# Performance work log

Hardware: AMD Instinct MI355X
Metric: run time of the kernel (lower is better)

Reference implementation:

```python
import jax, jax.numpy as jnp
import numpy as np

B, T, C = 4, 2048, 1024
NH = 16
HS = C // NH


def setup_inputs() -> dict:
    key = jax.random.key(0)
    k1, k2, k3, k4, k5 = jax.random.split(key, 5)
    scale = 1.0 / np.sqrt(C)
    return {
        "x": jax.random.normal(k1, (B, T, C), dtype=jnp.float32),
        "Wk": jax.random.normal(k2, (C, C), dtype=jnp.float32) * scale,
        "Wq": jax.random.normal(k3, (C, C), dtype=jnp.float32) * scale,
        "Wv": jax.random.normal(k4, (C, C), dtype=jnp.float32) * scale,
        "Wp": jax.random.normal(k5, (C, C), dtype=jnp.float32) * scale,
    }


def reference(x, Wk, Wq, Wv, Wp):
    b, t, c = x.shape
    # projections (nn.Linear with bias=False computes x @ W.T; weights here are
    # stored so that x @ W is equivalent -- same math, random init either way)
    k = (x @ Wk).reshape(b, t, NH, HS).transpose(0, 2, 1, 3)  # [B,H,T,hs]
    q = (x @ Wq).reshape(b, t, NH, HS).transpose(0, 2, 1, 3)
    v = (x @ Wv).reshape(b, t, NH, HS).transpose(0, 2, 1, 3)
    att = jnp.einsum("bhqd,bhkd->bhqk", q, k) / jnp.sqrt(jnp.float32(HS))
    causal = jnp.tril(jnp.ones((t, t), dtype=bool))
    att = jnp.where(causal[None, None, :, :], att, -jnp.inf)
    att = jax.nn.softmax(att, axis=-1)
    y = jnp.einsum("bhqk,bhkd->bhqd", att, v)  # [B,H,T,hs]
    y = y.transpose(0, 2, 1, 3).reshape(b, t, c)
    return y @ Wp
```

## Files before the change

### kernel.cpp

```cpp
#include <hip/hip_runtime.h>
#include <cstddef>
#include <cstdint>


namespace {

typedef unsigned short u16;
typedef unsigned int u32;
typedef __attribute__((ext_vector_type(8))) short s8v;
typedef __attribute__((ext_vector_type(4))) short s4v;
typedef __attribute__((ext_vector_type(4))) float f4v;

constexpr int Bn = 4, Tn = 2048, Cn = 1024;
constexpr int Mn = Bn * Tn;
constexpr int KVB = 128;
constexpr int NT128 = Tn / 128;
constexpr float QSCALE = 0.125f * 1.44269504f;

__device__ __forceinline__ u16 bfc(float f) {
  return __builtin_bit_cast(u16, (__bf16)f);
}

__device__ __forceinline__ f4v mfma16(s8v a, s8v b, f4v c) {
  return __builtin_amdgcn_mfma_f32_16x16x32_bf16(a, b, c, 0, 0, 0);
}

__device__ __forceinline__ f4v mfma16k16(s4v a, s4v b, f4v c) {
#if __has_builtin(__builtin_amdgcn_mfma_f32_16x16x16bf16_1k)
  return __builtin_amdgcn_mfma_f32_16x16x16bf16_1k(a, b, c, 0, 0, 0);
#else
  f4v d = c;
  asm("v_mfma_f32_16x16x16_bf16 %0, %1, %2, %0" : "+v"(d) : "v"(a), "v"(b));
  return d;
#endif
}

typedef __attribute__((address_space(1))) const u32 gas_u32;
typedef __attribute__((address_space(3))) u32 las_u32;
__device__ __forceinline__ void gl_lds16(const void* g, void* l) {
  __builtin_amdgcn_global_load_lds((gas_u32*)g, (las_u32*)l, 16, 0, 0);
}

__global__ __launch_bounds__(256) void cvtx(const float* __restrict__ in,
                                            u16* __restrict__ out) {
  const size_t i = ((size_t)blockIdx.x * 256 + threadIdx.x) * 8;
  const float4 a = *(const float4*)(in + i);
  const float4 b = *(const float4*)(in + i + 4);
  alignas(16) u16 t[8] = {bfc(a.x), bfc(a.y), bfc(a.z), bfc(a.w),
                          bfc(b.x), bfc(b.y), bfc(b.z), bfc(b.w)};
  *(s8v*)(out + i) = *(const s8v*)t;
}

__global__ __launch_bounds__(256) void wtrans(
    const float* __restrict__ w0, const float* __restrict__ w1,
    const float* __restrict__ w2, const float* __restrict__ w3,
    u16* __restrict__ o0, u16* __restrict__ o1, u16* __restrict__ o2,
    u16* __restrict__ o3) {
  const float* W;
  u16* O;
  switch (blockIdx.z) {
    case 0: W = w0; O = o0; break;
    case 1: W = w1; O = o1; break;
    case 2: W = w2; O = o2; break;
    default: W = w3; O = o3; break;
  }
  __shared__ float Tsh[64][65];
  const int tid = threadIdx.x;
  const int n0 = blockIdx.x * 64, k0 = blockIdx.y * 64;
  {
    const int rk = tid >> 2, c0 = (tid & 3) * 16;
#pragma unroll
    for (int u = 0; u < 4; ++u) {
      const float4 v = *(const float4*)&W[(size_t)(k0 + rk) * Cn + n0 + c0 + u * 4];
      Tsh[rk][c0 + u * 4 + 0] = v.x;
      Tsh[rk][c0 + u * 4 + 1] = v.y;
      Tsh[rk][c0 + u * 4 + 2] = v.z;
      Tsh[rk][c0 + u * 4 + 3] = v.w;
    }
  }
  __syncthreads();
  {
    const int rn = tid >> 2, ck0 = (tid & 3) * 16;
    alignas(16) u16 t[16];
#pragma unroll
    for (int u = 0; u < 16; ++u) t[u] = bfc(Tsh[ck0 + u][rn]);
    *(s8v*)&O[(size_t)(n0 + rn) * Cn + k0 + ck0] = *(const s8v*)&t[0];
    *(s8v*)&O[(size_t)(n0 + rn) * Cn + k0 + ck0 + 8] = *(const s8v*)&t[8];
  }
}

template <int OUT_MODE>
__device__ __forceinline__ void gemm_body(const u16* __restrict__ A,
                                          const u16* __restrict__ Bt,
                                          void* __restrict__ Cout, int bm,
                                          int bn, u16* As, u16* Bs) {
  const int N = Cn, K = Cn;
  const int tid = threadIdx.x;
  const int l = tid & 63, w = tid >> 6;
  const int lr = l & 15, lh = l >> 4;
  const int lrow = tid >> 2;
  const int lkcol = (tid & 3) * 8;
  const u16* Ag = A + (size_t)(bm * 128 + lrow) * K + lkcol;
  const u16* Bg = Bt + (size_t)(bn * 128 + lrow) * K + lkcol;
  const int wm = (w >> 1) * 64, wn = (w & 1) * 64;
  f4v acc[4][4] = {};
  for (int k0 = 0; k0 < K; k0 += 32) {
    __syncthreads();
    gl_lds16(Ag + k0, &As[(size_t)tid * 8]);
    gl_lds16(Ag + (size_t)64 * K + k0, &As[2048 + (size_t)tid * 8]);
    gl_lds16(Bg + k0, &Bs[(size_t)tid * 8]);
    gl_lds16(Bg + (size_t)64 * K + k0, &Bs[2048 + (size_t)tid * 8]);
    __syncthreads();
    s8v af[4], bfr[4];
#pragma unroll
    for (int i = 0; i < 4; ++i)
      af[i] = *(const s8v*)&As[(wm + i * 16 + lr) * 32 + lh * 8];
#pragma unroll
    for (int j = 0; j < 4; ++j)
      bfr[j] = *(const s8v*)&Bs[(wn + j * 16 + lr) * 32 + lh * 8];
    __builtin_amdgcn_s_setprio(1);
#pragma unroll
    for (int i = 0; i < 4; ++i)
#pragma unroll
      for (int j = 0; j < 4; ++j)
        acc[i][j] = mfma16(af[i], bfr[j], acc[i][j]);
    __builtin_amdgcn_s_setprio(0);
  }
  if (OUT_MODE == 2) {
    float* Cf = (float*)Cout;
#pragma unroll
    for (int i = 0; i < 4; ++i) {
      const int row = bm * 128 + wm + i * 16 + lh * 4;
#pragma unroll
      for (int j = 0; j < 4; ++j) {
        const int col = bn * 128 + wn + j * 16 + lr;
#pragma unroll
        for (int r = 0; r < 4; ++r)
          Cf[(size_t)(row + r) * N + col] = acc[i][j][r];
      }
    }
  } else if (OUT_MODE == 0 || OUT_MODE == 3) {
    u16* Cb = (u16*)Cout;
    const float sc = (OUT_MODE == 3) ? QSCALE : 1.0f;
#pragma unroll
    for (int i = 0; i < 4; ++i) {
      const int row = bm * 128 + wm + i * 16 + lh * 4;
#pragma unroll
      for (int j = 0; j < 4; ++j) {
        const int col = bn * 128 + wn + j * 16 + lr;
#pragma unroll
        for (int r = 0; r < 4; ++r)
          Cb[(size_t)(row + r) * N + col] = bfc(acc[i][j][r] * sc);
      }
    }
  } else {
    u16* Vt = (u16*)Cout;
#pragma unroll
    for (int i = 0; i < 4; ++i) {
      const int row0 = bm * 128 + wm + i * 16 + lh * 4;
      const int bq = row0 >> 11, t0 = row0 & 2047;
#pragma unroll
      for (int j = 0; j < 4; ++j) {
        const int col = bn * 128 + wn + j * 16 + lr;
        const int hh = col >> 6, dd = col & 63;
        alignas(8) u16 t4[4];
#pragma unroll
        for (int r = 0; r < 4; ++r) t4[r] = bfc(acc[i][j][r]);
        *(s4v*)&Vt[((size_t)((bq * 16 + hh) * 64 + dd)) * Tn + t0] =
            *(const s4v*)t4;
      }
    }
  }
}

__global__ __launch_bounds__(256) void gemm_qkv(
    const u16* __restrict__ A, const u16* __restrict__ btq,
    const u16* __restrict__ btk, const u16* __restrict__ btv,
    u16* __restrict__ qb, u16* __restrict__ kb, u16* __restrict__ vt) {
  __shared__ __align__(16) u16 As[4096], Bs[4096];
  const int bid = blockIdx.x;
  const int wg = (bid & 7) * 192 + (bid >> 3);
  const int which = wg >> 9, inner = wg & 511;
  const int bm = inner & 63, bn = inner >> 6;
  if (which == 0)
    gemm_body<3>(A, btq, qb, bm, bn, As, Bs);
  else if (which == 1)
    gemm_body<0>(A, btk, kb, bm, bn, As, Bs);
  else
    gemm_body<1>(A, btv, vt, bm, bn, As, Bs);
}

template <int OUT_MODE>
__global__ __launch_bounds__(256) void gemm_bt(const u16* __restrict__ A,
                                               const u16* __restrict__ Bt,
                                               void* __restrict__ Cout) {
  __shared__ __align__(16) u16 As[4096], Bs[4096];
  const int bid = blockIdx.x;
  const int wg = (bid & 7) * 64 + (bid >> 3);
  const int bm = wg & 63, bn = wg >> 6;
  gemm_body<OUT_MODE>(A, Bt, Cout, bm, bn, As, Bs);
}

__device__ __forceinline__ void attn_step(const s8v* aq, const u16* Ks,
                                          const u16* Vs, int ln, int w,
                                          int lr, int lh, bool diag, int k0,
                                          int q0, float& m_i, float& l_i,
                                          f4v* o) {
  f4v s[8] = {};
  {
    const int sw = lr & 7;
    __builtin_amdgcn_s_setprio(1);
#pragma unroll
    for (int n = 0; n < 8; ++n) {
      const int rk = n * 16 + lr;
#pragma unroll
      for (int kd = 0; kd < 2; ++kd) {
        const s8v bk = *(const s8v*)&Ks[rk * 64 + (((kd * 4 + lh) ^ sw) * 8)];
        s[n] = mfma16(bk, aq[kd], s[n]);
      }
    }
    __builtin_amdgcn_s_setprio(0);
  }
  const int qg = q0 + w * 16 + lr;
  float rm = -1e30f;
  if (diag) {
#pragma unroll
    for (int n = 0; n < 8; ++n)
#pragma unroll
      for (int r = 0; r < 4; ++r) {
        float x = s[n][r];
        if (k0 + n * 16 + lh * 4 + r > qg) x = -1e30f;
        s[n][r] = x;
        rm = fmaxf(rm, x);
      }
  } else {
#pragma unroll
    for (int n = 0; n < 8; ++n)
#pragma unroll
      for (int r = 0; r < 4; ++r) rm = fmaxf(rm, s[n][r]);
  }
  rm = fmaxf(rm, __shfl_xor(rm, 16));
  rm = fmaxf(rm, __shfl_xor(rm, 32));
  if (!__all(rm <= m_i + 11.5f)) {
    const float mnew = fmaxf(m_i, rm);
    const float al = exp2f(m_i - mnew);
    m_i = mnew;
    l_i *= al;
#pragma unroll
    for (int r = 0; r < 4; ++r) {
      const float ar = __shfl(al, (ln & 48) | (lh * 4 + r));
#pragma unroll
      for (int n2 = 0; n2 < 4; ++n2) o[n2][r] *= ar;
    }
  }
  float rs = 0.f;
#pragma unroll
  for (int n = 0; n < 8; ++n) {
    const float p0 = exp2f(s[n][0] - m_i);
    const float p1 = exp2f(s[n][1] - m_i);
    const float p2 = exp2f(s[n][2] - m_i);
    const float p3 = exp2f(s[n][3] - m_i);
    rs += (p0 + p1) + (p2 + p3);
    const s4v pa = {(short)bfc(p0), (short)bfc(p1), (short)bfc(p2),
                    (short)bfc(p3)};
    __builtin_amdgcn_s_setprio(1);
#pragma unroll
    for (int n2 = 0; n2 < 4; ++n2) {
      const int d = n2 * 16 + lr;
      const int cl = (2 * n + (lh >> 1)) ^ (lr & 7);
      const s4v bv = *(const s4v*)&Vs[d * 128 + cl * 8 + (lh & 1) * 4];
      o[n2] = mfma16k16(pa, bv, o[n2]);
    }
    __builtin_amdgcn_s_setprio(0);
  }
  rs += __shfl_xor(rs, 16);
  rs += __shfl_xor(rs, 32);
  l_i += rs;
}

__global__ __launch_bounds__(512) void attn_big(const u16* __restrict__ qg,
                                                const u16* __restrict__ kg,
                                                const u16* __restrict__ vtg,
                                                u16* __restrict__ yg) {
  __shared__ __align__(16) u16 Ks[KVB * 64];
  __shared__ __align__(16) u16 Vs[64 * KVB];
  const int tid = threadIdx.x;
  const int ln = tid & 63, w = tid >> 6;
  const int lr = ln & 15, lh = ln >> 4;
  const int bid = blockIdx.x;
  const int wg = (bid & 7) * 64 + (bid >> 3);
  const int bh = wg >> 3, xp = wg & 7;
  const int b = bh >> 4, h = bh & 15;
  const int tL = xp, tH = NT128 - 1 - xp;
  const int q0L = tL * 128, q0H = tH * 128;
  s8v aqL[2], aqH[2];
  {
    const int row = w * 16 + lr;
#pragma unroll
    for (int kd = 0; kd < 2; ++kd) {
      aqL[kd] = *(const s8v*)&qg[(size_t)(b * Tn + q0L + row) * Cn + h * 64 +
                                 kd * 32 + lh * 8];
      aqH[kd] = *(const s8v*)&qg[(size_t)(b * Tn + q0H + row) * Cn + h * 64 +
                                 kd * 32 + lh * 8];
    }
  }
  float mL = -1e30f, lL = 0.f, mH = -1e30f, lH = 0.f;
  f4v oL[4] = {}, oH[4] = {};
  const int krr0 = tid >> 3, krc = (tid & 7) * 8;
  const int vrr0 = tid >> 4, vrc = (tid & 15) * 8;
  s8v kr0, kr1, vr0, vr1;
  {
    kr0 = *(const s8v*)&kg[(size_t)(b * Tn + krr0) * Cn + h * 64 + krc];
    kr1 = *(const s8v*)&kg[(size_t)(b * Tn + 64 + krr0) * Cn + h * 64 + krc];
    vr0 = *(const s8v*)&vtg[((size_t)(bh * 64 + vrr0)) * Tn + vrc];
    vr1 = *(const s8v*)&vtg[((size_t)(bh * 64 + 32 + vrr0)) * Tn + vrc];
  }
  for (int kt = 0; kt <= tH; ++kt) {
    __syncthreads();
    {
      const int c = tid & 7;
      *(s8v*)&Ks[krr0 * 64 + ((c ^ (krr0 & 7)) * 8)] = kr0;
      *(s8v*)&Ks[(64 + krr0) * 64 + ((c ^ ((64 + krr0) & 7)) * 8)] = kr1;
      const int cv = tid & 15;
      *(s8v*)&Vs[vrr0 * 128 + ((cv ^ (vrr0 & 7)) * 8)] = vr0;
      *(s8v*)&Vs[(32 + vrr0) * 128 + ((cv ^ ((32 + vrr0) & 7)) * 8)] = vr1;
    }
    __syncthreads();
    if (kt < tH) {
      const int k0n = (kt + 1) * KVB;
      kr0 = *(const s8v*)&kg[(size_t)(b * Tn + k0n + krr0) * Cn + h * 64 + krc];
      kr1 = *(const s8v*)&kg[(size_t)(b * Tn + k0n + 64 + krr0) * Cn + h * 64 + krc];
      vr0 = *(const s8v*)&vtg[((size_t)(bh * 64 + vrr0)) * Tn + k0n + vrc];
      vr1 = *(const s8v*)&vtg[((size_t)(bh * 64 + 32 + vrr0)) * Tn + k0n + vrc];
    }
    attn_step(aqH, Ks, Vs, ln, w, lr, lh, kt == tH, kt * KVB, q0H, mH, lH, oH);
    if (kt <= tL)
      attn_step(aqL, Ks, Vs, ln, w, lr, lh, kt == tL, kt * KVB, q0L, mL, lL,
                oL);
  }
  {
    const float linv = 1.0f / lH;
#pragma unroll
    for (int r = 0; r < 4; ++r) {
      const float iv = __shfl(linv, (ln & 48) | (lh * 4 + r));
      const int row = q0H + w * 16 + lh * 4 + r;
#pragma unroll
      for (int n2 = 0; n2 < 4; ++n2)
        yg[(size_t)(b * Tn + row) * Cn + h * 64 + n2 * 16 + lr] =
            bfc(oH[n2][r] * iv);
    }
  }
  {
    const float linv = 1.0f / lL;
#pragma unroll
    for (int r = 0; r < 4; ++r) {
      const float iv = __shfl(linv, (ln & 48) | (lh * 4 + r));
      const int row = q0L + w * 16 + lh * 4 + r;
#pragma unroll
      for (int n2 = 0; n2 < 4; ++n2)
        yg[(size_t)(b * Tn + row) * Cn + h * 64 + n2 * 16 + lr] =
            bfc(oL[n2][r] * iv);
    }
  }
}

}

extern "C" void kernel_launch(void* const* d_in, const int* in_sizes, int n_in,
                              void* d_out, int out_size, void* d_ws,
                              size_t ws_size, hipStream_t stream) {
  (void)in_sizes; (void)n_in; (void)out_size; (void)ws_size;
  const float* x = (const float*)d_in[0];
  const float* Wk = (const float*)d_in[1];
  const float* Wq = (const float*)d_in[2];
  const float* Wv = (const float*)d_in[3];
  const float* Wp = (const float*)d_in[4];
  float* out = (float*)d_out;
  char* ws = (char*)d_ws;

  u16* xb = (u16*)(ws);
  u16* wqt = (u16*)(ws + 16777216);
  u16* wkt = (u16*)(ws + 18874368);
  u16* wvt = (u16*)(ws + 20971520);
  u16* wpt = (u16*)(ws + 23068672);
  u16* qb = (u16*)(ws + 25165824);
  u16* kb = (u16*)(ws + 41943040);
  u16* vt = (u16*)(ws + 58720256);
  u16* yb = (u16*)(ws + 75497472);

  cvtx<<<dim3(4096), dim3(256), 0, stream>>>(x, xb);
  wtrans<<<dim3(16, 16, 4), dim3(256), 0, stream>>>(Wq, Wk, Wv, Wp, wqt, wkt,
                                                    wvt, wpt);
  gemm_qkv<<<dim3(1536), dim3(256), 0, stream>>>(xb, wqt, wkt, wvt, qb, kb,
                                                 vt);
  attn_big<<<dim3(512), dim3(512), 0, stream>>>(qb, kb, vt, yb);
  gemm_bt<2><<<dim3(512), dim3(256), 0, stream>>>(yb, wpt, out);
}
```

Measured before the change: 209.1 us.

## Double-buffer K/V tiles with direct global-to-LDS loads and defer softmax reductions

Replaces the register-staged K/V load with double-buffered LDS tiles filled by direct global-to-LDS copies, so the next tile loads while the current one is computed and one barrier per iteration is dropped. Moves the row-sum cross-lane reduction to the epilogue and does the max shuffle only when a rescale is needed. Switches to the hardware exp2 intrinsic and adds an occupancy hint to launch bounds. Doubling LDS use may reduce occupancy, and the deferred per-lane max check changes when rescales happen.

```diff
diff --git a/kernel.cpp b/kernel.cpp
--- a/kernel.cpp
+++ b/kernel.cpp
@@ -19,6 +19,14 @@
 
 __device__ __forceinline__ u16 bfc(float f) {
   return __builtin_bit_cast(u16, (__bf16)f);
+}
+
+__device__ __forceinline__ float ex2(float x) {
+#if __has_builtin(__builtin_amdgcn_exp2f)
+  return __builtin_amdgcn_exp2f(x);
+#else
+  return exp2f(x);
+#endif
 }
 
 __device__ __forceinline__ f4v mfma16(s8v a, s8v b, f4v c) {
@@ -201,11 +209,32 @@
   gemm_body<OUT_MODE>(A, Bt, Cout, bm, bn, As, Bs);
 }
 
-__device__ __forceinline__ void attn_step(const s8v* aq, const u16* Ks,
-                                          const u16* Vs, int ln, int w,
-                                          int lr, int lh, bool diag, int k0,
-                                          int q0, float& m_i, float& l_i,
-                                          f4v* o) {
+__device__ __forceinline__ void stage_kv(const u16* __restrict__ kgb,
+                                         const u16* __restrict__ vtb,
+                                         u16* __restrict__ Kb,
+                                         u16* __restrict__ Vb, int k0,
+                                         int tid) {
+#pragma unroll
+  for (int is = 0; is < 2; ++is) {
+    const int slot = is * 512 + tid;
+    const int row = slot >> 3, ch = slot & 7;
+    gl_lds16(kgb + (size_t)(k0 + row) * Cn + ((ch ^ (row & 7)) * 8),
+             &Kb[slot * 8]);
+  }
+#pragma unroll
+  for (int is = 0; is < 2; ++is) {
+    const int slot = is * 512 + tid;
+    const int d = slot >> 4, ch = slot & 15;
+    gl_lds16(vtb + (size_t)d * Tn + k0 + ((ch ^ (d & 7)) * 8), &Vb[slot * 8]);
+  }
+}
+
+__device__ __forceinline__ void attn_step(const s8v* aq,
+                                          const u16* __restrict__ Ks,
+                                          const u16* __restrict__ Vs, int ln,
+                                          int w, int lr, int lh, bool diag,
+                                          int k0, int q0, float& m_i,
+                                          float& l_i, f4v* o) {
   f4v s[8] = {};
   {
     const int sw = lr & 7;
@@ -236,14 +265,13 @@
   } else {
 #pragma unroll
     for (int n = 0; n < 8; ++n)
-#pragma unroll
-      for (int r = 0; r < 4; ++r) rm = fmaxf(rm, s[n][r]);
-  }
-  rm = fmaxf(rm, __shfl_xor(rm, 16));
-  rm = fmaxf(rm, __shfl_xor(rm, 32));
+      rm = fmaxf(rm, fmaxf(fmaxf(s[n][0], s[n][1]), fmaxf(s[n][2], s[n][3])));
+  }
   if (!__all(rm <= m_i + 11.5f)) {
-    const float mnew = fmaxf(m_i, rm);
-    const float al = exp2f(m_i - mnew);
+    float rr = fmaxf(rm, __shfl_xor(rm, 16));
+    rr = fmaxf(rr, __shfl_xor(rr, 32));
+    const float mnew = fmaxf(m_i, rr);
+    const float al = ex2(m_i - mnew);
     m_i = mnew;
     l_i *= al;
 #pragma unroll
@@ -256,10 +284,10 @@
   float rs = 0.f;
 #pragma unroll
   for (int n = 0; n < 8; ++n) {
-    const float p0 = exp2f(s[n][0] - m_i);
-    const float p1 = exp2f(s[n][1] - m_i);
-    const float p2 = exp2f(s[n][2] - m_i);
-    const float p3 = exp2f(s[n][3] - m_i);
+    const float p0 = ex2(s[n][0] - m_i);
+    const float p1 = ex2(s[n][1] - m_i);
+    const float p2 = ex2(s[n][2] - m_i);
+    const float p3 = ex2(s[n][3] - m_i);
     rs += (p0 + p1) + (p2 + p3);
     const s4v pa = {(short)bfc(p0), (short)bfc(p1), (short)bfc(p2),
                     (short)bfc(p3)};
@@ -273,17 +301,14 @@
     }
     __builtin_amdgcn_s_setprio(0);
   }
-  rs += __shfl_xor(rs, 16);
-  rs += __shfl_xor(rs, 32);
   l_i += rs;
 }
 
-__global__ __launch_bounds__(512) void attn_big(const u16* __restrict__ qg,
-                                                const u16* __restrict__ kg,
-                                                const u16* __restrict__ vtg,
-                                                u16* __restrict__ yg) {
-  __shared__ __align__(16) u16 Ks[KVB * 64];
-  __shared__ __align__(16) u16 Vs[64 * KVB];
+__global__ __launch_bounds__(512, 4) void attn_big(
+    const u16* __restrict__ qg, const u16* __restrict__ kg,
+    const u16* __restrict__ vtg, u16* __restrict__ yg) {
+  __shared__ __align__(16) u16 Ks0[KVB * 64], Ks1[KVB * 64];
+  __shared__ __align__(16) u16 Vs0[64 * KVB], Vs1[64 * KVB];
   const int tid = threadIdx.x;
   const int ln = tid & 63, w = tid >> 6;
   const int lr = ln & 15, lh = ln >> 4;
@@ -293,6 +318,8 @@
   const int b = bh >> 4, h = bh & 15;
   const int tL = xp, tH = NT128 - 1 - xp;
   const int q0L = tL * 128, q0H = tH * 128;
+  const u16* kgb = kg + (size_t)(b * Tn) * Cn + h * 64;
+  const u16* vtb = vtg + (size_t)(bh * 64) * Tn;
   s8v aqL[2], aqH[2];
   {
     const int row = w * 16 + lr;
@@ -306,40 +333,27 @@
   }
   float mL = -1e30f, lL = 0.f, mH = -1e30f, lH = 0.f;
   f4v oL[4] = {}, oH[4] = {};
-  const int krr0 = tid >> 3, krc = (tid & 7) * 8;
-  const int vrr0 = tid >> 4, vrc = (tid & 15) * 8;
-  s8v kr0, kr1, vr0, vr1;
-  {
-    kr0 = *(const s8v*)&kg[(size_t)(b * Tn + krr0) * Cn + h * 64 + krc];
-    kr1 = *(const s8v*)&kg[(size_t)(b * Tn + 64 + krr0) * Cn + h * 64 + krc];
-    vr0 = *(const s8v*)&vtg[((size_t)(bh * 64 + vrr0)) * Tn + vrc];
-    vr1 = *(const s8v*)&vtg[((size_t)(bh * 64 + 32 + vrr0)) * Tn + vrc];
-  }
+  stage_kv(kgb, vtb, Ks0, Vs0, 0, tid);
+  __syncthreads();
   for (int kt = 0; kt <= tH; ++kt) {
+    const bool cur = kt & 1;
+    const u16* Kb = cur ? Ks1 : Ks0;
+    const u16* Vb = cur ? Vs1 : Vs0;
+    if (kt < tH)
+      stage_kv(kgb, vtb, cur ? Ks0 : Ks1, cur ? Vs0 : Vs1, (kt + 1) * KVB,
+               tid);
+    attn_step(aqH, Kb, Vb, ln, w, lr, lh, kt == tH, kt * KVB, q0H, mH, lH,
+              oH);
+    if (kt <= tL)
+      attn_step(aqL, Kb, Vb, ln, w, lr, lh, kt == tL, kt * KVB, q0L, mL, lL,
+                oL);
     __syncthreads();
-    {
-      const int c = tid & 7;
-      *(s8v*)&Ks[krr0 * 64 + ((c ^ (krr0 & 7)) * 8)] = kr0;
-      *(s8v*)&Ks[(64 + krr0) * 64 + ((c ^ ((64 + krr0) & 7)) * 8)] = kr1;
-      const int cv = tid & 15;
-      *(s8v*)&Vs[vrr0 * 128 + ((cv ^ (vrr0 & 7)) * 8)] = vr0;
-      *(s8v*)&Vs[(32 + vrr0) * 128 + ((cv ^ ((32 + vrr0) & 7)) * 8)] = vr1;
-    }
-    __syncthreads();
-    if (kt < tH) {
-      const int k0n = (kt + 1) * KVB;
-      kr0 = *(const s8v*)&kg[(size_t)(b * Tn + k0n + krr0) * Cn + h * 64 + krc];
-      kr1 = *(const s8v*)&kg[(size_t)(b * Tn + k0n + 64 + krr0) * Cn + h * 64 + krc];
-      vr0 = *(const s8v*)&vtg[((size_t)(bh * 64 + vrr0)) * Tn + k0n + vrc];
-      vr1 = *(const s8v*)&vtg[((size_t)(bh * 64 + 32 + vrr0)) * Tn + k0n + vrc];
-    }
-    attn_step(aqH, Ks, Vs, ln, w, lr, lh, kt == tH, kt * KVB, q0H, mH, lH, oH);
-    if (kt <= tL)
-      attn_step(aqL, Ks, Vs, ln, w, lr, lh, kt == tL, kt * KVB, q0L, mL, lL,
-                oL);
-  }
-  {
-    const float linv = 1.0f / lH;
+  }
+  {
+    float ls = lH;
+    ls += __shfl_xor(ls, 16);
+    ls += __shfl_xor(ls, 32);
+    const float linv = 1.0f / ls;
 #pragma unroll
     for (int r = 0; r < 4; ++r) {
       const float iv = __shfl(linv, (ln & 48) | (lh * 4 + r));
@@ -351,7 +365,10 @@
     }
   }
   {
-    const float linv = 1.0f / lL;
+    float ls = lL;
+    ls += __shfl_xor(ls, 16);
+    ls += __shfl_xor(ls, 32);
+    const float linv = 1.0f / ls;
 #pragma unroll
     for (int r = 0; r < 4; ++r) {
       const float iv = __shfl(linv, (ln & 48) | (lh * 4 + r));
```

New measurement: 257.8 us. 1.23x slower.
